# Optimization experiments

Measured on AMD Instinct MI355X. Metric: run time of the kernel, lower is better.

Reference implementation:

```python
import jax, jax.numpy as jnp
import numpy as np

H = 4            # heads
C = 64           # per-head dim (= hidden, PyG TransformerConv semantics)
HD = 64          # hidden_dim
L = 2            # num_layers
NT = 2           # node types: 0=task, 1=machine
ET = ((0, 1), (1, 0))  # edge types: (src_nt, dst_nt)
N = 16384        # nodes per type (== max_nodes -> simple pos-enc slice)
E = 262144       # edges per edge type


def _ln(x, g, b):
    mu = x.mean(-1, keepdims=True)
    var = ((x - mu) ** 2).mean(-1, keepdims=True)
    return (x - mu) * jax.lax.rsqrt(var + 1e-5) * g + b


def _tconv(x_src, x_dst, ei, Wq, bq, Wk, bk, Wv, bv, Ws, bs, Wb):
    # PyG TransformerConv: heads=H, out_channels=C, concat=False, beta=True
    n_dst = x_dst.shape[0]
    src, dst = ei[0], ei[1]
    q = (x_dst @ Wq + bq).reshape(-1, H, C)
    k = (x_src @ Wk + bk).reshape(-1, H, C)
    v = (x_src @ Wv + bv).reshape(-1, H, C)
    logits = jnp.einsum('ehc,ehc->eh', q[dst], k[src]) * (1.0 / float(np.sqrt(C)))  # [E,H]
    m = jax.ops.segment_max(logits, dst, num_segments=n_dst)          # [N,H] segment softmax
    ex = jnp.exp(logits - m[dst])
    denom = jax.ops.segment_sum(ex, dst, num_segments=n_dst)
    alpha = ex / denom[dst]                                            # [E,H]
    msg = (alpha[:, :, None] * v[src]).reshape(-1, H * C)              # [E,H*C]
    out = jax.ops.segment_sum(msg, dst, num_segments=n_dst)
    out = out.reshape(n_dst, H, C).mean(axis=1)                        # concat=False -> head mean
    r = x_dst @ Ws + bs                                                # lin_skip
    beta = jax.nn.sigmoid(jnp.concatenate([out, r, out - r], -1) @ Wb) # lin_beta, [N,1]
    return beta * r + (1.0 - beta) * out


def _forward(edge_index, x, W_in, b_in, type_emb, pos, Wq, bq, Wk, bk, Wv, bv,
             Wskip, bskip, Wbeta, ln_g, ln_b, ff_W1, ff_b1, ff_W2, ff_b2, W_out, b_out):
    # input proj + type embedding + positional encoding (num_nodes == max_nodes -> slice)
    h = [x[t] @ W_in[t] + b_in[t] + type_emb[t] + pos[t] for t in range(NT)]
    for l in range(L):
        hn = [jnp.zeros_like(h[0]), jnp.zeros_like(h[1])]
        for e, (s, d) in enumerate(ET):  # HeteroConv, aggr='sum'
            hn[d] = hn[d] + _tconv(h[s], h[d], edge_index[e],
                                   Wq[l, e], bq[l, e], Wk[l, e], bk[l, e],
                                   Wv[l, e], bv[l, e], Wskip[l, e], bskip[l, e], Wbeta[l, e])
        for t in range(NT):
            hr = _ln(h[t] + hn[t], ln_g[l, t], ln_b[l, t])
            ff = jax.nn.gelu(hr @ ff_W1[l, t] + ff_b1[l, t], approximate=False) @ ff_W2[l, t] + ff_b2[l, t]
            h[t] = hr + ff
    return jnp.stack([h[t] @ W_out[t] + b_out[t] for t in range(NT)])  # [NT,N,HD]


def setup_inputs() -> dict:
    key = jax.random.key(0)
    ks = jax.random.split(key, 16)
    w = lambda k, s: 0.02 * jax.random.normal(k, s, jnp.float32)
    NE = len(ET)
    return {
        'x': jax.random.normal(ks[0], (NT, N, HD), jnp.float32),
        'edge_index': jax.random.randint(ks[1], (NE, 2, E), 0, N, jnp.int32),
        'W_in': w(ks[2], (NT, HD, HD)), 'b_in': jnp.zeros((NT, HD), jnp.float32),
        'type_emb': w(ks[3], (NT, HD)),
        'pos': w(ks[4], (NT, N, HD)),
        'Wq': w(ks[5], (L, NE, HD, H * C)), 'bq': jnp.zeros((L, NE, H * C), jnp.float32),
        'Wk': w(ks[6], (L, NE, HD, H * C)), 'bk': jnp.zeros((L, NE, H * C), jnp.float32),
        'Wv': w(ks[7], (L, NE, HD, H * C)), 'bv': jnp.zeros((L, NE, H * C), jnp.float32),
        'Wskip': w(ks[8], (L, NE, HD, HD)), 'bskip': jnp.zeros((L, NE, HD), jnp.float32),
        'Wbeta': w(ks[9], (L, NE, 3 * HD, 1)),
        'ln_g': jnp.ones((L, NT, HD), jnp.float32), 'ln_b': jnp.zeros((L, NT, HD), jnp.float32),
        'ff_W1': w(ks[10], (L, NT, HD, 4 * HD)), 'ff_b1': jnp.zeros((L, NT, 4 * HD), jnp.float32),
        'ff_W2': w(ks[11], (L, NT, 4 * HD, HD)), 'ff_b2': jnp.zeros((L, NT, HD), jnp.float32),
        'W_out': w(ks[12], (NT, HD, HD)), 'b_out': jnp.zeros((NT, HD), jnp.float32),
    }


def reference(x, edge_index, W_in, b_in, type_emb, pos, Wq, bq, Wk, bk, Wv, bv,
              Wskip, bskip, Wbeta, ln_g, ln_b, ff_W1, ff_b1, ff_W2, ff_b2, W_out, b_out):
    return _forward(edge_index, x, W_in, b_in, type_emb, pos, Wq, bq, Wk, bk, Wv, bv,
                    Wskip, bskip, Wbeta, ln_g, ln_b, ff_W1, ff_b1, ff_W2, ff_b2, W_out, b_out)
```

## Files before the change

kernel.cpp:

```cpp
#include <hip/hip_runtime.h>
#include <math.h>

#define NN 16384
#define EE 262144

typedef __bf16 v8bf __attribute__((ext_vector_type(8)));
typedef __bf16 v4bf __attribute__((ext_vector_type(4)));
typedef float  v4f  __attribute__((ext_vector_type(4)));
typedef float  v2f  __attribute__((ext_vector_type(2)));

#define OFF_CNT     0
#define OFF_FILL    (2*NN)
#define OFF_ROWPTR  (4*NN)
#define OFF_COLSRC  98816
#define OFF_H       623104
#define OFF_HN      (OFF_H  + 2*NN*64)
#define OFF_Q       (OFF_HN + 2*NN*64)
#define OFF_KV      (OFF_Q  + 2*NN*128)
#define OFF_R       (OFF_KV + 2*NN*192)

__device__ __forceinline__ float blo(unsigned u) { return __uint_as_float(u << 16); }
__device__ __forceinline__ float bhi(unsigned u) { return __uint_as_float(u & 0xffff0000u); }
__device__ __forceinline__ unsigned short f2b(float f) {
  __bf16 h = (__bf16)f;
  return *(unsigned short*)&h;
}

__global__ void count_kernel(const int* __restrict__ ei, int* __restrict__ cnt) {
  int idx = blockIdx.x * 256 + threadIdx.x;
  if (idx >= 2 * EE) return;
  int et = idx >> 18;
  int j  = idx & (EE - 1);
  int dst = ei[et * 2 * EE + EE + j];
  atomicAdd(&cnt[et * NN + dst], 1);
}

__global__ __launch_bounds__(1024) void scan_kernel(const int* __restrict__ cnt,
                                                    int* __restrict__ rowptr,
                                                    int* __restrict__ fill) {
  int et = blockIdx.x;
  const int* c = cnt + et * NN;
  __shared__ int sums[1024];
  int tid = threadIdx.x;
  int base = tid * 16;
  int loc[16];
  int s = 0;
#pragma unroll
  for (int i = 0; i < 16; ++i) { loc[i] = s; s += c[base + i]; }
  sums[tid] = s;
  __syncthreads();
  for (int off = 1; off < 1024; off <<= 1) {
    int v = 0;
    if (tid >= off) v = sums[tid - off];
    __syncthreads();
    if (tid >= off) sums[tid] += v;
    __syncthreads();
  }
  int ebase = (tid == 0) ? 0 : sums[tid - 1];
  int* rp = rowptr + et * (NN + 1);
  int* fl = fill + et * NN;
#pragma unroll
  for (int i = 0; i < 16; ++i) {
    rp[base + i] = ebase + loc[i];
    fl[base + i] = ebase + loc[i];
  }
  if (tid == 1023) rp[NN] = sums[1023];
}

__global__ void scatter_kernel(const int* __restrict__ ei, int* __restrict__ fill,
                               int* __restrict__ colsrc) {
  int idx = blockIdx.x * 256 + threadIdx.x;
  if (idx >= 2 * EE) return;
  int et = idx >> 18;
  int j  = idx & (EE - 1);
  int src = ei[et * 2 * EE + j];
  int dst = ei[et * 2 * EE + EE + j];
  int pos = atomicAdd(&fill[et * NN + dst], 1);
  colsrc[et * EE + pos] = (et * NN + src) * 768;
}

struct GemmDesc {
  const float *A, *B, *bias, *bias2, *add;
  char* C;
  int K, Ncols, Cld, tile0, ntiles, gelu, otype;
};
struct GemmPack { GemmDesc d[8]; int nd; };

#define LDA 72

__global__ __launch_bounds__(256) void gemm_mfma(GemmPack p) {
  int y = blockIdx.y;
  int di = 0;
  for (int i = 0; i < p.nd; ++i)
    if (y >= p.d[i].tile0 && y < p.d[i].tile0 + p.d[i].ntiles) di = i;
  GemmDesc g = p.d[di];
  const int col0 = (y - g.tile0) * 64;
  const int row0 = blockIdx.x * 128;
  const int tid = threadIdx.x;
  const int w = tid >> 6, lane = tid & 63;
  const int l16 = lane & 15, quad = lane >> 4;

  __shared__ __bf16 As[128 * LDA];
  __shared__ __bf16 Bs[64 * LDA];

  v4f acc[2][4];
#pragma unroll
  for (int rt = 0; rt < 2; ++rt)
#pragma unroll
    for (int ct = 0; ct < 4; ++ct)
#pragma unroll
      for (int r = 0; r < 4; ++r) acc[rt][ct][r] = 0.f;

  for (int kt = 0; kt < g.K; kt += 64) {
#pragma unroll
    for (int it = 0; it < 8; ++it) {
      int fi = it * 256 + tid;
      int grow = fi >> 4;
      int kq = (fi & 15) << 2;
      float4 a = *(const float4*)(g.A + (size_t)(row0 + grow) * g.K + kt + kq);
      v4bf c = { (__bf16)a.x, (__bf16)a.y, (__bf16)a.z, (__bf16)a.w };
      *(v4bf*)&As[grow * LDA + kq] = c;
    }
#pragma unroll
    for (int it = 0; it < 4; ++it) {
      int fi = it * 256 + tid;
      int kk = fi >> 4;
      int nq = (fi & 15) << 2;
      float4 b = *(const float4*)(g.B + (size_t)(kt + kk) * g.Ncols + col0 + nq);
      Bs[(nq + 0) * LDA + kk] = (__bf16)b.x;
      Bs[(nq + 1) * LDA + kk] = (__bf16)b.y;
      Bs[(nq + 2) * LDA + kk] = (__bf16)b.z;
      Bs[(nq + 3) * LDA + kk] = (__bf16)b.w;
    }
    __syncthreads();
#pragma unroll
    for (int ks = 0; ks < 2; ++ks) {
      v8bf a0 = *(v8bf*)&As[(w * 32 + l16) * LDA + ks * 32 + quad * 8];
      v8bf a1 = *(v8bf*)&As[(w * 32 + 16 + l16) * LDA + ks * 32 + quad * 8];
#pragma unroll
      for (int ct = 0; ct < 4; ++ct) {
        v8bf bb = *(v8bf*)&Bs[(ct * 16 + l16) * LDA + ks * 32 + quad * 8];
        acc[0][ct] = __builtin_amdgcn_mfma_f32_16x16x32_bf16(a0, bb, acc[0][ct], 0, 0, 0);
        acc[1][ct] = __builtin_amdgcn_mfma_f32_16x16x32_bf16(a1, bb, acc[1][ct], 0, 0, 0);
      }
    }
    __syncthreads();
  }

  float bias_c[4];
#pragma unroll
  for (int ct = 0; ct < 4; ++ct) {
    int col = col0 + ct * 16 + l16;
    float b = g.bias ? g.bias[col] : 0.f;
    if (g.bias2) b += g.bias2[col];
    bias_c[ct] = b;
  }
#pragma unroll
  for (int rt = 0; rt < 2; ++rt)
#pragma unroll
    for (int r = 0; r < 4; ++r) {
      size_t row = row0 + w * 32 + rt * 16 + quad * 4 + r;
      char* cp = g.C + row * (size_t)g.Cld;
#pragma unroll
      for (int ct = 0; ct < 4; ++ct) {
        int col = col0 + ct * 16 + l16;
        float v = acc[rt][ct][r] + bias_c[ct];
        if (g.add) v += g.add[row * g.Ncols + col];
        if (g.gelu) v = 0.5f * v * (1.f + erff(v * 0.70710678118654752f));
        if (g.otype == 0)      *(float*)(cp + col * 4) = v;
        else if (g.otype == 1) *(unsigned short*)(cp + col * 2) = f2b(v);
        else {
          unsigned pk = __builtin_amdgcn_cvt_pk_fp8_f32(v, v, 0, false);
          *(unsigned char*)(cp + col) = (unsigned char)(pk & 0xff);
        }
      }
    }
}

struct FFPack {
  const float *HN, *W1, *b1, *W2, *b2;
  float* H;
};

__global__ __launch_bounds__(256) void ff_fused(FFPack p) {
  const int t = blockIdx.y;
  const int row0 = blockIdx.x * 64;
  const int tid = threadIdx.x;
  const int w = tid >> 6, lane = tid & 63;
  const int l16 = lane & 15, quad = lane >> 4;

  const float* A  = p.HN + ((size_t)t * NN) * 64;
  const float* W1 = p.W1 + (size_t)t * 64 * 256;
  const float* b1 = p.b1 + t * 256;
  const float* W2 = p.W2 + (size_t)t * 256 * 64;
  const float* b2 = p.b2 + t * 64;

  __shared__ __bf16 As[64 * LDA];
  __shared__ __bf16 A2[64 * LDA];
  __shared__ __bf16 B1s[64 * LDA];
  __shared__ __bf16 B2s[64 * LDA];

#pragma unroll
  for (int it = 0; it < 4; ++it) {
    int fi = it * 256 + tid;
    int grow = fi >> 4;
    int kq = (fi & 15) << 2;
    float4 a = *(const float4*)(A + (size_t)(row0 + grow) * 64 + kq);
    v4bf c = { (__bf16)a.x, (__bf16)a.y, (__bf16)a.z, (__bf16)a.w };
    *(v4bf*)&As[grow * LDA + kq] = c;
  }

  v4f acc2[4];
#pragma unroll
  for (int ct = 0; ct < 4; ++ct)
#pragma unroll
    for (int r = 0; r < 4; ++r) acc2[ct][r] = 0.f;

  for (int c1 = 0; c1 < 4; ++c1) {
#pragma unroll
    for (int it = 0; it < 4; ++it) {
      int fi = it * 256 + tid;
      int kk = fi >> 4;
      int nq = (fi & 15) << 2;
      float4 b = *(const float4*)(W1 + (size_t)kk * 256 + c1 * 64 + nq);
      B1s[(nq + 0) * LDA + kk] = (__bf16)b.x;
      B1s[(nq + 1) * LDA + kk] = (__bf16)b.y;
      B1s[(nq + 2) * LDA + kk] = (__bf16)b.z;
      B1s[(nq + 3) * LDA + kk] = (__bf16)b.w;
      float4 b2v = *(const float4*)(W2 + (size_t)(c1 * 64 + kk) * 64 + nq);
      B2s[(nq + 0) * LDA + kk] = (__bf16)b2v.x;
      B2s[(nq + 1) * LDA + kk] = (__bf16)b2v.y;
      B2s[(nq + 2) * LDA + kk] = (__bf16)b2v.z;
      B2s[(nq + 3) * LDA + kk] = (__bf16)b2v.w;
    }
    __syncthreads();

    v4f acc1[4];
#pragma unroll
    for (int ct = 0; ct < 4; ++ct)
#pragma unroll
      for (int r = 0; r < 4; ++r) acc1[ct][r] = 0.f;
#pragma unroll
    for (int ks = 0; ks < 2; ++ks) {
      v8bf a = *(v8bf*)&As[(w * 16 + l16) * LDA + ks * 32 + quad * 8];
#pragma unroll
      for (int ct = 0; ct < 4; ++ct) {
        v8bf bb = *(v8bf*)&B1s[(ct * 16 + l16) * LDA + ks * 32 + quad * 8];
        acc1[ct] = __builtin_amdgcn_mfma_f32_16x16x32_bf16(a, bb, acc1[ct], 0, 0, 0);
      }
    }
#pragma unroll
    for (int ct = 0; ct < 4; ++ct) {
      float bb = b1[c1 * 64 + ct * 16 + l16];
#pragma unroll
      for (int r = 0; r < 4; ++r) {
        float v = acc1[ct][r] + bb;
        v = 0.5f * v * (1.f + erff(v * 0.70710678118654752f));
        A2[(w * 16 + quad * 4 + r) * LDA + ct * 16 + l16] = (__bf16)v;
      }
    }
#pragma unroll
    for (int ks = 0; ks < 2; ++ks) {
      v8bf a = *(v8bf*)&A2[(w * 16 + l16) * LDA + ks * 32 + quad * 8];
#pragma unroll
      for (int ct = 0; ct < 4; ++ct) {
        v8bf bb = *(v8bf*)&B2s[(ct * 16 + l16) * LDA + ks * 32 + quad * 8];
        acc2[ct] = __builtin_amdgcn_mfma_f32_16x16x32_bf16(a, bb, acc2[ct], 0, 0, 0);
      }
    }
    __syncthreads();
  }

#pragma unroll
  for (int ct = 0; ct < 4; ++ct) {
    int col = ct * 16 + l16;
    float bb = b2[col];
#pragma unroll
    for (int r = 0; r < 4; ++r) {
      size_t row = (size_t)t * NN + row0 + w * 16 + quad * 4 + r;
      float v = acc2[ct][r] + bb + p.HN[row * 64 + col];
      p.H[row * 64 + col] = v;
    }
  }
}

struct AggPack {
  const unsigned short *Q;
  const char *KV;
  const float *R;
  const float *Wb;
  const float *Hin;
  const float *lng, *lnb;
  float* outHR;
  const int *rowptr;
  const int *colsrc;
};

__global__ __launch_bounds__(256) void agg_kernel(AggPack p) {
  const int et = blockIdx.y, d = 1 - et;
  int wid = __builtin_amdgcn_readfirstlane(threadIdx.x >> 6);
  int lane = threadIdx.x & 63;
  int node = blockIdx.x * 4 + wid;
  int c4 = lane & 15;
  int cb = ((lane >> 4) << 6) + (c4 << 2);

  const int* rp = p.rowptr + et * (NN + 1);
  const int* cs = p.colsrc + et * EE;
  int start = rp[node], end = rp[node + 1];
  int len = end - start;
  int gnode = d * NN + node;

  uint2 qw = *(const uint2*)(p.Q + ((size_t)gnode << 8) + cb);
  float q0 = blo(qw.x) * 0.125f, q1 = bhi(qw.x) * 0.125f;
  float q2 = blo(qw.y) * 0.125f, q3 = bhi(qw.y) * 0.125f;

  int b[5];
#pragma unroll
  for (int i = 0; i <= 4; ++i) b[i] = start + ((len * i) >> 2);
  float dsum[4] = {0.f, 0.f, 0.f, 0.f};
  float acc[4][4];
#pragma unroll
  for (int s4 = 0; s4 < 4; ++s4)
#pragma unroll
    for (int c = 0; c < 4; ++c) acc[s4][c] = 0.f;

  int maxn = (len + 3) >> 2;
  int last = end - 1;
  for (int it = 0; it < maxn; ++it) {
#pragma unroll
    for (int s4 = 0; s4 < 4; ++s4) {
      int j = b[s4] + it;
      bool act = j < b[s4 + 1];
      int jc = act ? j : last;
      int off = cs[jc];
      const char* rowp = p.KV + off;
      unsigned kw = *(const unsigned*)(rowp + cb);
      uint2 vw = *(const uint2*)(rowp + 256 + cb * 2);
      v2f kl = __builtin_amdgcn_cvt_pk_f32_fp8((int)kw, false);
      v2f kh = __builtin_amdgcn_cvt_pk_f32_fp8((int)kw, true);
      float pd = q0 * kl[0] + q1 * kl[1] + q2 * kh[0] + q3 * kh[1];
      pd += __shfl_xor(pd, 1);
      pd += __shfl_xor(pd, 2);
      pd += __shfl_xor(pd, 4);
      pd += __shfl_xor(pd, 8);
      float wgt = act ? __expf(pd) : 0.f;
      dsum[s4] += wgt;
      acc[s4][0] += wgt * blo(vw.x);
      acc[s4][1] += wgt * bhi(vw.x);
      acc[s4][2] += wgt * blo(vw.y);
      acc[s4][3] += wgt * bhi(vw.y);
    }
  }
  float dn = (dsum[0] + dsum[1]) + (dsum[2] + dsum[3]);
  float ax = (acc[0][0] + acc[1][0]) + (acc[2][0] + acc[3][0]);
  float ay = (acc[0][1] + acc[1][1]) + (acc[2][1] + acc[3][1]);
  float az = (acc[0][2] + acc[1][2]) + (acc[2][2] + acc[3][2]);
  float aw = (acc[0][3] + acc[1][3]) + (acc[2][3] + acc[3][3]);

  float inv = (len > 0) ? (0.25f / dn) : 0.f;
  float ox = ax * inv, oy = ay * inv, oz = az * inv, ow = aw * inv;
  ox += __shfl_xor(ox, 16); ox += __shfl_xor(ox, 32);
  oy += __shfl_xor(oy, 16); oy += __shfl_xor(oy, 32);
  oz += __shfl_xor(oz, 16); oz += __shfl_xor(oz, 32);
  ow += __shfl_xor(ow, 16); ow += __shfl_xor(ow, 32);

  int cc = c4 << 2;
  float4 r = *(const float4*)(p.R + (size_t)gnode * 64 + cc);
  const float* wb = p.Wb + et * 192;
  float part = ox * wb[cc] + oy * wb[cc + 1] + oz * wb[cc + 2] + ow * wb[cc + 3]
             + r.x * wb[64 + cc] + r.y * wb[64 + cc + 1]
             + r.z * wb[64 + cc + 2] + r.w * wb[64 + cc + 3]
             + (ox - r.x) * wb[128 + cc] + (oy - r.y) * wb[128 + cc + 1]
             + (oz - r.z) * wb[128 + cc + 2] + (ow - r.w) * wb[128 + cc + 3];
  part += __shfl_xor(part, 1);
  part += __shfl_xor(part, 2);
  part += __shfl_xor(part, 4);
  part += __shfl_xor(part, 8);
  float beta = 1.f / (1.f + __expf(-part));

  float4 hv = *(const float4*)(p.Hin + (size_t)gnode * 64 + cc);
  float yx = hv.x + beta * r.x + (1.f - beta) * ox;
  float yy = hv.y + beta * r.y + (1.f - beta) * oy;
  float yz = hv.z + beta * r.z + (1.f - beta) * oz;
  float yw = hv.w + beta * r.w + (1.f - beta) * ow;
  float sa = yx + yy + yz + yw;
  float sb = yx * yx + yy * yy + yz * yz + yw * yw;
  sa += __shfl_xor(sa, 1); sb += __shfl_xor(sb, 1);
  sa += __shfl_xor(sa, 2); sb += __shfl_xor(sb, 2);
  sa += __shfl_xor(sa, 4); sb += __shfl_xor(sb, 4);
  sa += __shfl_xor(sa, 8); sb += __shfl_xor(sb, 8);
  float mu = sa * (1.f / 64.f);
  float var = sb * (1.f / 64.f) - mu * mu;
  float rs = rsqrtf(var + 1e-5f);
  if (lane < 16) {
    const float* lng = p.lng + d * 64;
    const float* lnb = p.lnb + d * 64;
    float4 gg = *(const float4*)(lng + cc);
    float4 bb = *(const float4*)(lnb + cc);
    float4 res;
    res.x = (yx - mu) * rs * gg.x + bb.x;
    res.y = (yy - mu) * rs * gg.y + bb.y;
    res.z = (yz - mu) * rs * gg.z + bb.z;
    res.w = (yw - mu) * rs * gg.w + bb.w;
    *(float4*)(p.outHR + (size_t)gnode * 64 + cc) = res;
  }
}

static void add_desc(GemmPack& p, int& tiles, const float* A, const float* B,
                     const float* bias, const float* bias2, const float* add,
                     void* C, int K, int Nc, int Cld, int gelu, int otype) {
  GemmDesc& g = p.d[p.nd++];
  g.A = A; g.B = B; g.bias = bias; g.bias2 = bias2; g.add = add; g.C = (char*)C;
  g.K = K; g.Ncols = Nc; g.Cld = Cld; g.tile0 = tiles; g.ntiles = Nc / 64;
  g.gelu = gelu; g.otype = otype;
  tiles += g.ntiles;
}

extern "C" void kernel_launch(void* const* d_in, const int* in_sizes, int n_in,
                              void* d_out, int out_size, void* d_ws, size_t ws_size,
                              hipStream_t stream) {
  const float* x        = (const float*)d_in[0];
  const int*   ei       = (const int*)d_in[1];
  const float* W_in     = (const float*)d_in[2];
  const float* b_in     = (const float*)d_in[3];
  const float* type_emb = (const float*)d_in[4];
  const float* pos      = (const float*)d_in[5];
  const float* Wq       = (const float*)d_in[6];
  const float* bq       = (const float*)d_in[7];
  const float* Wk       = (const float*)d_in[8];
  const float* bk       = (const float*)d_in[9];
  const float* Wv       = (const float*)d_in[10];
  const float* bv       = (const float*)d_in[11];
  const float* Wskip    = (const float*)d_in[12];
  const float* bskip    = (const float*)d_in[13];
  const float* Wbeta    = (const float*)d_in[14];
  const float* ln_g     = (const float*)d_in[15];
  const float* ln_b     = (const float*)d_in[16];
  const float* ff_W1    = (const float*)d_in[17];
  const float* ff_b1    = (const float*)d_in[18];
  const float* ff_W2    = (const float*)d_in[19];
  const float* ff_b2    = (const float*)d_in[20];
  const float* W_out    = (const float*)d_in[21];
  const float* b_out    = (const float*)d_in[22];
  float* out = (float*)d_out;

  int*   wsi = (int*)d_ws;
  float* wsf = (float*)d_ws;
  int* cnt    = wsi + OFF_CNT;
  int* fill   = wsi + OFF_FILL;
  int* rowptr = wsi + OFF_ROWPTR;
  int* colsrc = wsi + OFF_COLSRC;
  float* H  = wsf + OFF_H;
  float* HN = wsf + OFF_HN;
  unsigned short* Qb = (unsigned short*)(wsf + OFF_Q);
  char* KVb = (char*)(wsf + OFF_KV);
  float* Rb = wsf + OFF_R;

  hipMemsetAsync(cnt, 0, 2 * NN * sizeof(int), stream);
  count_kernel<<<dim3(2 * EE / 256), dim3(256), 0, stream>>>(ei, cnt);
  scan_kernel<<<dim3(2), dim3(1024), 0, stream>>>(cnt, rowptr, fill);
  scatter_kernel<<<dim3(2 * EE / 256), dim3(256), 0, stream>>>(ei, fill, colsrc);

  {
    GemmPack p{}; int tiles = 0;
    for (int t = 0; t < 2; ++t)
      add_desc(p, tiles, x + (size_t)t * NN * 64, W_in + t * 64 * 64,
               b_in + t * 64, type_emb + t * 64, pos + (size_t)t * NN * 64,
               H + (size_t)t * NN * 64, 64, 64, 256, 0, 0);
    gemm_mfma<<<dim3(128, tiles), dim3(256), 0, stream>>>(p);
  }

  for (int l = 0; l < 2; ++l) {
    {
      GemmPack p{}; int tiles = 0;
      for (int et = 0; et < 2; ++et) {
        int s = et, d = 1 - et;
        int we = l * 2 + et;
        const float* hs = H + (size_t)s * NN * 64;
        const float* hd = H + (size_t)d * NN * 64;
        add_desc(p, tiles, hd, Wq + (size_t)we * 64 * 256, bq + we * 256,
                 nullptr, nullptr, (char*)Qb + (size_t)d * NN * 512, 64, 256, 512, 0, 1);
        add_desc(p, tiles, hs, Wk + (size_t)we * 64 * 256, bk + we * 256,
                 nullptr, nullptr, KVb + (size_t)s * NN * 768, 64, 256, 768, 0, 2);
        add_desc(p, tiles, hs, Wv + (size_t)we * 64 * 256, bv + we * 256,
                 nullptr, nullptr, KVb + (size_t)s * NN * 768 + 256, 64, 256, 768, 0, 1);
        add_desc(p, tiles, hd, Wskip + (size_t)we * 64 * 64, bskip + we * 64,
                 nullptr, nullptr, Rb + (size_t)d * NN * 64, 64, 64, 256, 0, 0);
      }
      gemm_mfma<<<dim3(128, tiles), dim3(256), 0, stream>>>(p);
    }

    AggPack ap;
    ap.Q = Qb; ap.KV = KVb; ap.R = Rb;
    ap.Wb = Wbeta + l * 2 * 192;
    ap.Hin = H;
    ap.lng = ln_g + l * 128;
    ap.lnb = ln_b + l * 128;
    ap.outHR = HN;
    ap.rowptr = rowptr;
    ap.colsrc = colsrc;
    agg_kernel<<<dim3(NN / 4, 2), dim3(256), 0, stream>>>(ap);

    FFPack fp;
    fp.HN = HN;
    fp.W1 = ff_W1 + (size_t)l * 2 * 64 * 256;
    fp.b1 = ff_b1 + l * 2 * 256;
    fp.W2 = ff_W2 + (size_t)l * 2 * 256 * 64;
    fp.b2 = ff_b2 + l * 2 * 64;
    fp.H  = H;
    ff_fused<<<dim3(NN / 64, 2), dim3(256), 0, stream>>>(fp);
  }

  {
    GemmPack p{}; int tiles = 0;
    for (int t = 0; t < 2; ++t)
      add_desc(p, tiles, H + (size_t)t * NN * 64, W_out + t * 64 * 64,
               b_out + t * 64, nullptr, nullptr,
               out + (size_t)t * NN * 64, 64, 64, 256, 0, 0);
    gemm_mfma<<<dim3(128, tiles), dim3(256), 0, stream>>>(p);
  }
}
```

Baseline: 394.6 us.

## Reuse staged A tile across column tiles in GEMM; widen per-lane aggregation to 8 channels

The packed GEMM now launches one block per descriptor and row tile, stages the A rows into LDS once, and loops over all 64-column output tiles. Before, each column tile re-read and re-converted A. This cuts repeated global reads of the input activations but makes far fewer blocks (grid y shrinks from 26 to 8 in the projection launch) and serializes column tiles within a block. The aggregation kernel switches each lane to 8 channels with two half-waves processing two edge segments each. That gives wider K/V loads and fewer shuffle steps, at the cost of more registers per lane.

```diff
diff --git a/kernel.cpp b/kernel.cpp
--- a/kernel.cpp
+++ b/kernel.cpp
@@ -82,19 +82,14 @@
 struct GemmDesc {
   const float *A, *B, *bias, *bias2, *add;
   char* C;
-  int K, Ncols, Cld, tile0, ntiles, gelu, otype;
+  int Ncols, Cld, ntiles, gelu, otype;
 };
 struct GemmPack { GemmDesc d[8]; int nd; };
 
 #define LDA 72
 
 __global__ __launch_bounds__(256) void gemm_mfma(GemmPack p) {
-  int y = blockIdx.y;
-  int di = 0;
-  for (int i = 0; i < p.nd; ++i)
-    if (y >= p.d[i].tile0 && y < p.d[i].tile0 + p.d[i].ntiles) di = i;
-  GemmDesc g = p.d[di];
-  const int col0 = (y - g.tile0) * 64;
+  GemmDesc g = p.d[blockIdx.y];
   const int row0 = blockIdx.x * 128;
   const int tid = threadIdx.x;
   const int w = tid >> 6, lane = tid & 63;
@@ -103,36 +98,40 @@
   __shared__ __bf16 As[128 * LDA];
   __shared__ __bf16 Bs[64 * LDA];
 
-  v4f acc[2][4];
-#pragma unroll
-  for (int rt = 0; rt < 2; ++rt)
-#pragma unroll
-    for (int ct = 0; ct < 4; ++ct)
-#pragma unroll
-      for (int r = 0; r < 4; ++r) acc[rt][ct][r] = 0.f;
-
-  for (int kt = 0; kt < g.K; kt += 64) {
-#pragma unroll
-    for (int it = 0; it < 8; ++it) {
-      int fi = it * 256 + tid;
-      int grow = fi >> 4;
-      int kq = (fi & 15) << 2;
-      float4 a = *(const float4*)(g.A + (size_t)(row0 + grow) * g.K + kt + kq);
-      v4bf c = { (__bf16)a.x, (__bf16)a.y, (__bf16)a.z, (__bf16)a.w };
-      *(v4bf*)&As[grow * LDA + kq] = c;
-    }
+#pragma unroll
+  for (int it = 0; it < 8; ++it) {
+    int fi = it * 256 + tid;
+    int grow = fi >> 4;
+    int kq = (fi & 15) << 2;
+    float4 a = *(const float4*)(g.A + (size_t)(row0 + grow) * 64 + kq);
+    v4bf c = { (__bf16)a.x, (__bf16)a.y, (__bf16)a.z, (__bf16)a.w };
+    *(v4bf*)&As[grow * LDA + kq] = c;
+  }
+
+  for (int ct0 = 0; ct0 < g.ntiles; ++ct0) {
+    const int col0 = ct0 * 64;
+    __syncthreads();
 #pragma unroll
     for (int it = 0; it < 4; ++it) {
       int fi = it * 256 + tid;
       int kk = fi >> 4;
       int nq = (fi & 15) << 2;
-      float4 b = *(const float4*)(g.B + (size_t)(kt + kk) * g.Ncols + col0 + nq);
+      float4 b = *(const float4*)(g.B + (size_t)kk * g.Ncols + col0 + nq);
       Bs[(nq + 0) * LDA + kk] = (__bf16)b.x;
       Bs[(nq + 1) * LDA + kk] = (__bf16)b.y;
       Bs[(nq + 2) * LDA + kk] = (__bf16)b.z;
       Bs[(nq + 3) * LDA + kk] = (__bf16)b.w;
     }
     __syncthreads();
+
+    v4f acc[2][4];
+#pragma unroll
+    for (int rt = 0; rt < 2; ++rt)
+#pragma unroll
+      for (int ct = 0; ct < 4; ++ct)
+#pragma unroll
+        for (int r = 0; r < 4; ++r) acc[rt][ct][r] = 0.f;
+
 #pragma unroll
     for (int ks = 0; ks < 2; ++ks) {
       v8bf a0 = *(v8bf*)&As[(w * 32 + l16) * LDA + ks * 32 + quad * 8];
@@ -144,37 +143,36 @@
         acc[1][ct] = __builtin_amdgcn_mfma_f32_16x16x32_bf16(a1, bb, acc[1][ct], 0, 0, 0);
       }
     }
-    __syncthreads();
-  }
-
-  float bias_c[4];
-#pragma unroll
-  for (int ct = 0; ct < 4; ++ct) {
-    int col = col0 + ct * 16 + l16;
-    float b = g.bias ? g.bias[col] : 0.f;
-    if (g.bias2) b += g.bias2[col];
-    bias_c[ct] = b;
-  }
-#pragma unroll
-  for (int rt = 0; rt < 2; ++rt)
-#pragma unroll
-    for (int r = 0; r < 4; ++r) {
-      size_t row = row0 + w * 32 + rt * 16 + quad * 4 + r;
-      char* cp = g.C + row * (size_t)g.Cld;
-#pragma unroll
-      for (int ct = 0; ct < 4; ++ct) {
-        int col = col0 + ct * 16 + l16;
-        float v = acc[rt][ct][r] + bias_c[ct];
-        if (g.add) v += g.add[row * g.Ncols + col];
-        if (g.gelu) v = 0.5f * v * (1.f + erff(v * 0.70710678118654752f));
-        if (g.otype == 0)      *(float*)(cp + col * 4) = v;
-        else if (g.otype == 1) *(unsigned short*)(cp + col * 2) = f2b(v);
-        else {
-          unsigned pk = __builtin_amdgcn_cvt_pk_fp8_f32(v, v, 0, false);
-          *(unsigned char*)(cp + col) = (unsigned char)(pk & 0xff);
+
+    float bias_c[4];
+#pragma unroll
+    for (int ct = 0; ct < 4; ++ct) {
+      int col = col0 + ct * 16 + l16;
+      float b = g.bias ? g.bias[col] : 0.f;
+      if (g.bias2) b += g.bias2[col];
+      bias_c[ct] = b;
+    }
+#pragma unroll
+    for (int rt = 0; rt < 2; ++rt)
+#pragma unroll
+      for (int r = 0; r < 4; ++r) {
+        size_t row = row0 + w * 32 + rt * 16 + quad * 4 + r;
+        char* cp = g.C + row * (size_t)g.Cld;
+#pragma unroll
+        for (int ct = 0; ct < 4; ++ct) {
+          int col = col0 + ct * 16 + l16;
+          float v = acc[rt][ct][r] + bias_c[ct];
+          if (g.add) v += g.add[row * g.Ncols + col];
+          if (g.gelu) v = 0.5f * v * (1.f + erff(v * 0.70710678118654752f));
+          if (g.otype == 0)      *(float*)(cp + col * 4) = v;
+          else if (g.otype == 1) *(unsigned short*)(cp + col * 2) = f2b(v);
+          else {
+            unsigned pk = __builtin_amdgcn_cvt_pk_fp8_f32(v, v, 0, false);
+            *(unsigned char*)(cp + col) = (unsigned char)(pk & 0xff);
+          }
         }
       }
-    }
+  }
 }
 
 struct FFPack {
@@ -301,8 +299,10 @@
   int wid = __builtin_amdgcn_readfirstlane(threadIdx.x >> 6);
   int lane = threadIdx.x & 63;
   int node = blockIdx.x * 4 + wid;
-  int c4 = lane & 15;
-  int cb = ((lane >> 4) << 6) + (c4 << 2);
+  int lane5 = lane & 31;
+  int sub = lane >> 5;
+  int c8 = lane5 & 7;
+  int cb8 = ((lane5 >> 3) << 6) + (c8 << 3);
 
   const int* rp = p.rowptr + et * (NN + 1);
   const int* cs = p.colsrc + et * EE;
@@ -310,110 +310,141 @@
   int len = end - start;
   int gnode = d * NN + node;
 
-  uint2 qw = *(const uint2*)(p.Q + ((size_t)gnode << 8) + cb);
-  float q0 = blo(qw.x) * 0.125f, q1 = bhi(qw.x) * 0.125f;
-  float q2 = blo(qw.y) * 0.125f, q3 = bhi(qw.y) * 0.125f;
+  float q[8];
+  {
+    uint4 qw = *(const uint4*)(p.Q + ((size_t)gnode << 8) + cb8);
+    q[0] = blo(qw.x) * 0.125f; q[1] = bhi(qw.x) * 0.125f;
+    q[2] = blo(qw.y) * 0.125f; q[3] = bhi(qw.y) * 0.125f;
+    q[4] = blo(qw.z) * 0.125f; q[5] = bhi(qw.z) * 0.125f;
+    q[6] = blo(qw.w) * 0.125f; q[7] = bhi(qw.w) * 0.125f;
+  }
 
   int b[5];
 #pragma unroll
   for (int i = 0; i <= 4; ++i) b[i] = start + ((len * i) >> 2);
-  float dsum[4] = {0.f, 0.f, 0.f, 0.f};
-  float acc[4][4];
-#pragma unroll
-  for (int s4 = 0; s4 < 4; ++s4)
-#pragma unroll
-    for (int c = 0; c < 4; ++c) acc[s4][c] = 0.f;
+  int s0lo = sub ? b[2] : b[0];
+  int s0hi = sub ? b[3] : b[1];
+  int s1lo = sub ? b[3] : b[1];
+  int s1hi = sub ? b[4] : b[2];
+
+  float dsum[2] = {0.f, 0.f};
+  float acc[2][8];
+#pragma unroll
+  for (int u = 0; u < 2; ++u)
+#pragma unroll
+    for (int i = 0; i < 8; ++i) acc[u][i] = 0.f;
 
   int maxn = (len + 3) >> 2;
   int last = end - 1;
   for (int it = 0; it < maxn; ++it) {
 #pragma unroll
-    for (int s4 = 0; s4 < 4; ++s4) {
-      int j = b[s4] + it;
-      bool act = j < b[s4 + 1];
+    for (int u = 0; u < 2; ++u) {
+      int jlo = u ? s1lo : s0lo;
+      int jhi = u ? s1hi : s0hi;
+      int j = jlo + it;
+      bool act = j < jhi;
       int jc = act ? j : last;
       int off = cs[jc];
       const char* rowp = p.KV + off;
-      unsigned kw = *(const unsigned*)(rowp + cb);
-      uint2 vw = *(const uint2*)(rowp + 256 + cb * 2);
-      v2f kl = __builtin_amdgcn_cvt_pk_f32_fp8((int)kw, false);
-      v2f kh = __builtin_amdgcn_cvt_pk_f32_fp8((int)kw, true);
-      float pd = q0 * kl[0] + q1 * kl[1] + q2 * kh[0] + q3 * kh[1];
+      uint2 kw = *(const uint2*)(rowp + cb8);
+      uint4 vw = *(const uint4*)(rowp + 256 + cb8 * 2);
+      v2f k0 = __builtin_amdgcn_cvt_pk_f32_fp8((int)kw.x, false);
+      v2f k1 = __builtin_amdgcn_cvt_pk_f32_fp8((int)kw.x, true);
+      v2f k2 = __builtin_amdgcn_cvt_pk_f32_fp8((int)kw.y, false);
+      v2f k3 = __builtin_amdgcn_cvt_pk_f32_fp8((int)kw.y, true);
+      float pd = q[0] * k0[0] + q[1] * k0[1] + q[2] * k1[0] + q[3] * k1[1]
+               + q[4] * k2[0] + q[5] * k2[1] + q[6] * k3[0] + q[7] * k3[1];
       pd += __shfl_xor(pd, 1);
       pd += __shfl_xor(pd, 2);
       pd += __shfl_xor(pd, 4);
-      pd += __shfl_xor(pd, 8);
       float wgt = act ? __expf(pd) : 0.f;
-      dsum[s4] += wgt;
-      acc[s4][0] += wgt * blo(vw.x);
-      acc[s4][1] += wgt * bhi(vw.x);
-      acc[s4][2] += wgt * blo(vw.y);
-      acc[s4][3] += wgt * bhi(vw.y);
-    }
-  }
-  float dn = (dsum[0] + dsum[1]) + (dsum[2] + dsum[3]);
-  float ax = (acc[0][0] + acc[1][0]) + (acc[2][0] + acc[3][0]);
-  float ay = (acc[0][1] + acc[1][1]) + (acc[2][1] + acc[3][1]);
-  float az = (acc[0][2] + acc[1][2]) + (acc[2][2] + acc[3][2]);
-  float aw = (acc[0][3] + acc[1][3]) + (acc[2][3] + acc[3][3]);
-
+      dsum[u] += wgt;
+      acc[u][0] += wgt * blo(vw.x); acc[u][1] += wgt * bhi(vw.x);
+      acc[u][2] += wgt * blo(vw.y); acc[u][3] += wgt * bhi(vw.y);
+      acc[u][4] += wgt * blo(vw.z); acc[u][5] += wgt * bhi(vw.z);
+      acc[u][6] += wgt * blo(vw.w); acc[u][7] += wgt * bhi(vw.w);
+    }
+  }
+
+  float dn = dsum[0] + dsum[1];
+  dn += __shfl_xor(dn, 32);
+  float o[8];
+#pragma unroll
+  for (int i = 0; i < 8; ++i) {
+    float a = acc[0][i] + acc[1][i];
+    a += __shfl_xor(a, 32);
+    o[i] = a;
+  }
   float inv = (len > 0) ? (0.25f / dn) : 0.f;
-  float ox = ax * inv, oy = ay * inv, oz = az * inv, ow = aw * inv;
-  ox += __shfl_xor(ox, 16); ox += __shfl_xor(ox, 32);
-  oy += __shfl_xor(oy, 16); oy += __shfl_xor(oy, 32);
-  oz += __shfl_xor(oz, 16); oz += __shfl_xor(oz, 32);
-  ow += __shfl_xor(ow, 16); ow += __shfl_xor(ow, 32);
-
-  int cc = c4 << 2;
-  float4 r = *(const float4*)(p.R + (size_t)gnode * 64 + cc);
+#pragma unroll
+  for (int i = 0; i < 8; ++i) {
+    float v = o[i] * inv;
+    v += __shfl_xor(v, 8);
+    v += __shfl_xor(v, 16);
+    o[i] = v;
+  }
+
+  int cc = c8 << 3;
   const float* wb = p.Wb + et * 192;
-  float part = ox * wb[cc] + oy * wb[cc + 1] + oz * wb[cc + 2] + ow * wb[cc + 3]
-             + r.x * wb[64 + cc] + r.y * wb[64 + cc + 1]
-             + r.z * wb[64 + cc + 2] + r.w * wb[64 + cc + 3]
-             + (ox - r.x) * wb[128 + cc] + (oy - r.y) * wb[128 + cc + 1]
-             + (oz - r.z) * wb[128 + cc + 2] + (ow - r.w) * wb[128 + cc + 3];
+  float4 w0a = *(const float4*)(wb + cc),       w0b = *(const float4*)(wb + cc + 4);
+  float4 w1a = *(const float4*)(wb + 64 + cc),  w1b = *(const float4*)(wb + 64 + cc + 4);
+  float4 w2a = *(const float4*)(wb + 128 + cc), w2b = *(const float4*)(wb + 128 + cc + 4);
+  float4 ra = *(const float4*)(p.R + (size_t)gnode * 64 + cc);
+  float4 rb = *(const float4*)(p.R + (size_t)gnode * 64 + cc + 4);
+  float r[8] = {ra.x, ra.y, ra.z, ra.w, rb.x, rb.y, rb.z, rb.w};
+  float wb0[8] = {w0a.x, w0a.y, w0a.z, w0a.w, w0b.x, w0b.y, w0b.z, w0b.w};
+  float wb1[8] = {w1a.x, w1a.y, w1a.z, w1a.w, w1b.x, w1b.y, w1b.z, w1b.w};
+  float wb2[8] = {w2a.x, w2a.y, w2a.z, w2a.w, w2b.x, w2b.y, w2b.z, w2b.w};
+
+  float part = 0.f;
+#pragma unroll
+  for (int i = 0; i < 8; ++i)
+    part += o[i] * wb0[i] + r[i] * wb1[i] + (o[i] - r[i]) * wb2[i];
   part += __shfl_xor(part, 1);
   part += __shfl_xor(part, 2);
   part += __shfl_xor(part, 4);
-  part += __shfl_xor(part, 8);
   float beta = 1.f / (1.f + __expf(-part));
 
-  float4 hv = *(const float4*)(p.Hin + (size_t)gnode * 64 + cc);
-  float yx = hv.x + beta * r.x + (1.f - beta) * ox;
-  float yy = hv.y + beta * r.y + (1.f - beta) * oy;
-  float yz = hv.z + beta * r.z + (1.f - beta) * oz;
-  float yw = hv.w + beta * r.w + (1.f - beta) * ow;
-  float sa = yx + yy + yz + yw;
-  float sb = yx * yx + yy * yy + yz * yz + yw * yw;
+  float4 ha = *(const float4*)(p.Hin + (size_t)gnode * 64 + cc);
+  float4 hb = *(const float4*)(p.Hin + (size_t)gnode * 64 + cc + 4);
+  float hv[8] = {ha.x, ha.y, ha.z, ha.w, hb.x, hb.y, hb.z, hb.w};
+  float y[8];
+  float sa = 0.f, sb = 0.f;
+#pragma unroll
+  for (int i = 0; i < 8; ++i) {
+    y[i] = hv[i] + beta * r[i] + (1.f - beta) * o[i];
+    sa += y[i];
+    sb += y[i] * y[i];
+  }
   sa += __shfl_xor(sa, 1); sb += __shfl_xor(sb, 1);
   sa += __shfl_xor(sa, 2); sb += __shfl_xor(sb, 2);
   sa += __shfl_xor(sa, 4); sb += __shfl_xor(sb, 4);
-  sa += __shfl_xor(sa, 8); sb += __shfl_xor(sb, 8);
   float mu = sa * (1.f / 64.f);
   float var = sb * (1.f / 64.f) - mu * mu;
   float rs = rsqrtf(var + 1e-5f);
-  if (lane < 16) {
+  if (lane < 8) {
     const float* lng = p.lng + d * 64;
     const float* lnb = p.lnb + d * 64;
-    float4 gg = *(const float4*)(lng + cc);
-    float4 bb = *(const float4*)(lnb + cc);
-    float4 res;
-    res.x = (yx - mu) * rs * gg.x + bb.x;
-    res.y = (yy - mu) * rs * gg.y + bb.y;
-    res.z = (yz - mu) * rs * gg.z + bb.z;
-    res.w = (yw - mu) * rs * gg.w + bb.w;
-    *(float4*)(p.outHR + (size_t)gnode * 64 + cc) = res;
-  }
-}
-
-static void add_desc(GemmPack& p, int& tiles, const float* A, const float* B,
+    float4 ga = *(const float4*)(lng + cc), gb = *(const float4*)(lng + cc + 4);
+    float4 ba = *(const float4*)(lnb + cc), bbv = *(const float4*)(lnb + cc + 4);
+    float gg[8] = {ga.x, ga.y, ga.z, ga.w, gb.x, gb.y, gb.z, gb.w};
+    float bbx[8] = {ba.x, ba.y, ba.z, ba.w, bbv.x, bbv.y, bbv.z, bbv.w};
+    float res[8];
+#pragma unroll
+    for (int i = 0; i < 8; ++i) res[i] = (y[i] - mu) * rs * gg[i] + bbx[i];
+    float* op = p.outHR + (size_t)gnode * 64 + cc;
+    *(float4*)op = make_float4(res[0], res[1], res[2], res[3]);
+    *(float4*)(op + 4) = make_float4(res[4], res[5], res[6], res[7]);
+  }
+}
+
+static void add_desc(GemmPack& p, const float* A, const float* B,
                      const float* bias, const float* bias2, const float* add,
-                     void* C, int K, int Nc, int Cld, int gelu, int otype) {
+                     void* C, int Nc, int Cld, int gelu, int otype) {
   GemmDesc& g = p.d[p.nd++];
   g.A = A; g.B = B; g.bias = bias; g.bias2 = bias2; g.add = add; g.C = (char*)C;
-  g.K = K; g.Ncols = Nc; g.Cld = Cld; g.tile0 = tiles; g.ntiles = Nc / 64;
+  g.Ncols = Nc; g.Cld = Cld; g.ntiles = Nc / 64;
   g.gelu = gelu; g.otype = otype;
-  tiles += g.ntiles;
 }
 
 extern "C" void kernel_launch(void* const* d_in, const int* in_sizes, int n_in,
@@ -462,32 +493,32 @@
   scatter_kernel<<<dim3(2 * EE / 256), dim3(256), 0, stream>>>(ei, fill, colsrc);
 
   {
-    GemmPack p{}; int tiles = 0;
+    GemmPack p{};
     for (int t = 0; t < 2; ++t)
-      add_desc(p, tiles, x + (size_t)t * NN * 64, W_in + t * 64 * 64,
+      add_desc(p, x + (size_t)t * NN * 64, W_in + t * 64 * 64,
                b_in + t * 64, type_emb + t * 64, pos + (size_t)t * NN * 64,
-               H + (size_t)t * NN * 64, 64, 64, 256, 0, 0);
-    gemm_mfma<<<dim3(128, tiles), dim3(256), 0, stream>>>(p);
+               H + (size_t)t * NN * 64, 64, 256, 0, 0);
+    gemm_mfma<<<dim3(128, p.nd), dim3(256), 0, stream>>>(p);
   }
 
   for (int l = 0; l < 2; ++l) {
     {
-      GemmPack p{}; int tiles = 0;
+      GemmPack p{};
       for (int et = 0; et < 2; ++et) {
         int s = et, d = 1 - et;
         int we = l * 2 + et;
         const float* hs = H + (size_t)s * NN * 64;
         const float* hd = H + (size_t)d * NN * 64;
-        add_desc(p, tiles, hd, Wq + (size_t)we * 64 * 256, bq + we * 256,
-                 nullptr, nullptr, (char*)Qb + (size_t)d * NN * 512, 64, 256, 512, 0, 1);
-        add_desc(p, tiles, hs, Wk + (size_t)we * 64 * 256, bk + we * 256,
-                 nullptr, nullptr, KVb + (size_t)s * NN * 768, 64, 256, 768, 0, 2);
-        add_desc(p, tiles, hs, Wv + (size_t)we * 64 * 256, bv + we * 256,
-                 nullptr, nullptr, KVb + (size_t)s * NN * 768 + 256, 64, 256, 768, 0, 1);
-        add_desc(p, tiles, hd, Wskip + (size_t)we * 64 * 64, bskip + we * 64,
-                 nullptr, nullptr, Rb + (size_t)d * NN * 64, 64, 64, 256, 0, 0);
+        add_desc(p, hd, Wq + (size_t)we * 64 * 256, bq + we * 256,
+                 nullptr, nullptr, (char*)Qb + (size_t)d * NN * 512, 256, 512, 0, 1);
+        add_desc(p, hs, Wk + (size_t)we * 64 * 256, bk + we * 256,
+                 nullptr, nullptr, KVb + (size_t)s * NN * 768, 256, 768, 0, 2);
+        add_desc(p, hs, Wv + (size_t)we * 64 * 256, bv + we * 256,
+                 nullptr, nullptr, KVb + (size_t)s * NN * 768 + 256, 256, 768, 0, 1);
+        add_desc(p, hd, Wskip + (size_t)we * 64 * 64, bskip + we * 64,
+                 nullptr, nullptr, Rb + (size_t)d * NN * 64, 64, 256, 0, 0);
       }
-      gemm_mfma<<<dim3(128, tiles), dim3(256), 0, stream>>>(p);
+      gemm_mfma<<<dim3(128, p.nd), dim3(256), 0, stream>>>(p);
     }
 
     AggPack ap;
@@ -512,11 +543,11 @@
   }
 
   {
-    GemmPack p{}; int tiles = 0;
+    GemmPack p{};
     for (int t = 0; t < 2; ++t)
-      add_desc(p, tiles, H + (size_t)t * NN * 64, W_out + t * 64 * 64,
+      add_desc(p, H + (size_t)t * NN * 64, W_out + t * 64 * 64,
                b_out + t * 64, nullptr, nullptr,
-               out + (size_t)t * NN * 64, 64, 64, 256, 0, 0);
-    gemm_mfma<<<dim3(128, tiles), dim3(256), 0, stream>>>(p);
-  }
-}
+               out + (size_t)t * NN * 64, 64, 256, 0, 0);
+    gemm_mfma<<<dim3(128, p.nd), dim3(256), 0, stream>>>(p);
+  }
+}
```

Result: no change. 401.7 us (+1.8%).

## Reuse A tile across column tiles in GEMM and fuse output projection into FF

Applied to the files above, without the earlier changes.

The grouped GEMM now launches one block per descriptor instead of per 64-column tile. Each block loads and converts its 128-row A tile once, then loops over all column tiles, which removes redundant A reads for the wide Q/K/V projections. Separately, the final layer's FF kernel keeps the residual output in shared memory and applies the output projection there, so the last GEMM launch and the write and re-read of H are gone. The cost is fewer blocks in the QKV GEMM (8x128 instead of 26x128) and serialized column tiles per block, which can lower parallelism.

```diff
diff --git a/kernel.cpp b/kernel.cpp
--- a/kernel.cpp
+++ b/kernel.cpp
@@ -82,19 +82,14 @@
 struct GemmDesc {
   const float *A, *B, *bias, *bias2, *add;
   char* C;
-  int K, Ncols, Cld, tile0, ntiles, gelu, otype;
+  int Ncols, Cld, ntiles, gelu, otype;
 };
 struct GemmPack { GemmDesc d[8]; int nd; };
 
 #define LDA 72
 
 __global__ __launch_bounds__(256) void gemm_mfma(GemmPack p) {
-  int y = blockIdx.y;
-  int di = 0;
-  for (int i = 0; i < p.nd; ++i)
-    if (y >= p.d[i].tile0 && y < p.d[i].tile0 + p.d[i].ntiles) di = i;
-  GemmDesc g = p.d[di];
-  const int col0 = (y - g.tile0) * 64;
+  GemmDesc g = p.d[blockIdx.y];
   const int row0 = blockIdx.x * 128;
   const int tid = threadIdx.x;
   const int w = tid >> 6, lane = tid & 63;
@@ -103,36 +98,40 @@
   __shared__ __bf16 As[128 * LDA];
   __shared__ __bf16 Bs[64 * LDA];
 
-  v4f acc[2][4];
-#pragma unroll
-  for (int rt = 0; rt < 2; ++rt)
-#pragma unroll
-    for (int ct = 0; ct < 4; ++ct)
-#pragma unroll
-      for (int r = 0; r < 4; ++r) acc[rt][ct][r] = 0.f;
-
-  for (int kt = 0; kt < g.K; kt += 64) {
-#pragma unroll
-    for (int it = 0; it < 8; ++it) {
-      int fi = it * 256 + tid;
-      int grow = fi >> 4;
-      int kq = (fi & 15) << 2;
-      float4 a = *(const float4*)(g.A + (size_t)(row0 + grow) * g.K + kt + kq);
-      v4bf c = { (__bf16)a.x, (__bf16)a.y, (__bf16)a.z, (__bf16)a.w };
-      *(v4bf*)&As[grow * LDA + kq] = c;
-    }
+#pragma unroll
+  for (int it = 0; it < 8; ++it) {
+    int fi = it * 256 + tid;
+    int grow = fi >> 4;
+    int kq = (fi & 15) << 2;
+    float4 a = *(const float4*)(g.A + (size_t)(row0 + grow) * 64 + kq);
+    v4bf c = { (__bf16)a.x, (__bf16)a.y, (__bf16)a.z, (__bf16)a.w };
+    *(v4bf*)&As[grow * LDA + kq] = c;
+  }
+
+  for (int ct0 = 0; ct0 < g.ntiles; ++ct0) {
+    const int col0 = ct0 * 64;
+    __syncthreads();
 #pragma unroll
     for (int it = 0; it < 4; ++it) {
       int fi = it * 256 + tid;
       int kk = fi >> 4;
       int nq = (fi & 15) << 2;
-      float4 b = *(const float4*)(g.B + (size_t)(kt + kk) * g.Ncols + col0 + nq);
+      float4 b = *(const float4*)(g.B + (size_t)kk * g.Ncols + col0 + nq);
       Bs[(nq + 0) * LDA + kk] = (__bf16)b.x;
       Bs[(nq + 1) * LDA + kk] = (__bf16)b.y;
       Bs[(nq + 2) * LDA + kk] = (__bf16)b.z;
       Bs[(nq + 3) * LDA + kk] = (__bf16)b.w;
     }
     __syncthreads();
+
+    v4f acc[2][4];
+#pragma unroll
+    for (int rt = 0; rt < 2; ++rt)
+#pragma unroll
+      for (int ct = 0; ct < 4; ++ct)
+#pragma unroll
+        for (int r = 0; r < 4; ++r) acc[rt][ct][r] = 0.f;
+
 #pragma unroll
     for (int ks = 0; ks < 2; ++ks) {
       v8bf a0 = *(v8bf*)&As[(w * 32 + l16) * LDA + ks * 32 + quad * 8];
@@ -144,42 +143,43 @@
         acc[1][ct] = __builtin_amdgcn_mfma_f32_16x16x32_bf16(a1, bb, acc[1][ct], 0, 0, 0);
       }
     }
-    __syncthreads();
-  }
-
-  float bias_c[4];
-#pragma unroll
-  for (int ct = 0; ct < 4; ++ct) {
-    int col = col0 + ct * 16 + l16;
-    float b = g.bias ? g.bias[col] : 0.f;
-    if (g.bias2) b += g.bias2[col];
-    bias_c[ct] = b;
-  }
-#pragma unroll
-  for (int rt = 0; rt < 2; ++rt)
-#pragma unroll
-    for (int r = 0; r < 4; ++r) {
-      size_t row = row0 + w * 32 + rt * 16 + quad * 4 + r;
-      char* cp = g.C + row * (size_t)g.Cld;
-#pragma unroll
-      for (int ct = 0; ct < 4; ++ct) {
-        int col = col0 + ct * 16 + l16;
-        float v = acc[rt][ct][r] + bias_c[ct];
-        if (g.add) v += g.add[row * g.Ncols + col];
-        if (g.gelu) v = 0.5f * v * (1.f + erff(v * 0.70710678118654752f));
-        if (g.otype == 0)      *(float*)(cp + col * 4) = v;
-        else if (g.otype == 1) *(unsigned short*)(cp + col * 2) = f2b(v);
-        else {
-          unsigned pk = __builtin_amdgcn_cvt_pk_fp8_f32(v, v, 0, false);
-          *(unsigned char*)(cp + col) = (unsigned char)(pk & 0xff);
+
+    float bias_c[4];
+#pragma unroll
+    for (int ct = 0; ct < 4; ++ct) {
+      int col = col0 + ct * 16 + l16;
+      float b = g.bias ? g.bias[col] : 0.f;
+      if (g.bias2) b += g.bias2[col];
+      bias_c[ct] = b;
+    }
+#pragma unroll
+    for (int rt = 0; rt < 2; ++rt)
+#pragma unroll
+      for (int r = 0; r < 4; ++r) {
+        size_t row = row0 + w * 32 + rt * 16 + quad * 4 + r;
+        char* cp = g.C + row * (size_t)g.Cld;
+#pragma unroll
+        for (int ct = 0; ct < 4; ++ct) {
+          int col = col0 + ct * 16 + l16;
+          float v = acc[rt][ct][r] + bias_c[ct];
+          if (g.add) v += g.add[row * g.Ncols + col];
+          if (g.gelu) v = 0.5f * v * (1.f + erff(v * 0.70710678118654752f));
+          if (g.otype == 0)      *(float*)(cp + col * 4) = v;
+          else if (g.otype == 1) *(unsigned short*)(cp + col * 2) = f2b(v);
+          else {
+            unsigned pk = __builtin_amdgcn_cvt_pk_fp8_f32(v, v, 0, false);
+            *(unsigned char*)(cp + col) = (unsigned char)(pk & 0xff);
+          }
         }
       }
-    }
+  }
 }
 
 struct FFPack {
   const float *HN, *W1, *b1, *W2, *b2;
   float* H;
+  const float *Wout, *bout;
+  float* outbuf;
 };
 
 __global__ __launch_bounds__(256) void ff_fused(FFPack p) {
@@ -271,15 +271,72 @@
     __syncthreads();
   }
 
+  if (!p.outbuf) {
+#pragma unroll
+    for (int ct = 0; ct < 4; ++ct) {
+      int col = ct * 16 + l16;
+      float bb = b2[col];
+#pragma unroll
+      for (int r = 0; r < 4; ++r) {
+        size_t row = (size_t)t * NN + row0 + w * 16 + quad * 4 + r;
+        float v = acc2[ct][r] + bb + p.HN[row * 64 + col];
+        p.H[row * 64 + col] = v;
+      }
+    }
+    return;
+  }
+
 #pragma unroll
   for (int ct = 0; ct < 4; ++ct) {
     int col = ct * 16 + l16;
     float bb = b2[col];
 #pragma unroll
     for (int r = 0; r < 4; ++r) {
+      int lrow = w * 16 + quad * 4 + r;
+      size_t row = (size_t)t * NN + row0 + lrow;
+      float v = acc2[ct][r] + bb + p.HN[row * 64 + col];
+      A2[lrow * LDA + col] = (__bf16)v;
+    }
+  }
+  {
+    const float* Wo = p.Wout + (size_t)t * 64 * 64;
+#pragma unroll
+    for (int it = 0; it < 4; ++it) {
+      int fi = it * 256 + tid;
+      int kk = fi >> 4;
+      int nq = (fi & 15) << 2;
+      float4 b = *(const float4*)(Wo + (size_t)kk * 64 + nq);
+      B1s[(nq + 0) * LDA + kk] = (__bf16)b.x;
+      B1s[(nq + 1) * LDA + kk] = (__bf16)b.y;
+      B1s[(nq + 2) * LDA + kk] = (__bf16)b.z;
+      B1s[(nq + 3) * LDA + kk] = (__bf16)b.w;
+    }
+  }
+  __syncthreads();
+
+  v4f acc3[4];
+#pragma unroll
+  for (int ct = 0; ct < 4; ++ct)
+#pragma unroll
+    for (int r = 0; r < 4; ++r) acc3[ct][r] = 0.f;
+#pragma unroll
+  for (int ks = 0; ks < 2; ++ks) {
+    v8bf a = *(v8bf*)&A2[(w * 16 + l16) * LDA + ks * 32 + quad * 8];
+#pragma unroll
+    for (int ct = 0; ct < 4; ++ct) {
+      v8bf bb = *(v8bf*)&B1s[(ct * 16 + l16) * LDA + ks * 32 + quad * 8];
+      acc3[ct] = __builtin_amdgcn_mfma_f32_16x16x32_bf16(a, bb, acc3[ct], 0, 0, 0);
+    }
+  }
+  const float* bo = p.bout + t * 64;
+#pragma unroll
+  for (int ct = 0; ct < 4; ++ct) {
+    int col = ct * 16 + l16;
+    float bb = bo[col];
+#pragma unroll
+    for (int r = 0; r < 4; ++r) {
       size_t row = (size_t)t * NN + row0 + w * 16 + quad * 4 + r;
-      float v = acc2[ct][r] + bb + p.HN[row * 64 + col];
-      p.H[row * 64 + col] = v;
+      p.outbuf[row * 64 + col] = acc3[ct][r] + bb;
     }
   }
 }
@@ -406,14 +463,13 @@
   }
 }
 
-static void add_desc(GemmPack& p, int& tiles, const float* A, const float* B,
+static void add_desc(GemmPack& p, const float* A, const float* B,
                      const float* bias, const float* bias2, const float* add,
-                     void* C, int K, int Nc, int Cld, int gelu, int otype) {
+                     void* C, int Nc, int Cld, int gelu, int otype) {
   GemmDesc& g = p.d[p.nd++];
   g.A = A; g.B = B; g.bias = bias; g.bias2 = bias2; g.add = add; g.C = (char*)C;
-  g.K = K; g.Ncols = Nc; g.Cld = Cld; g.tile0 = tiles; g.ntiles = Nc / 64;
+  g.Ncols = Nc; g.Cld = Cld; g.ntiles = Nc / 64;
   g.gelu = gelu; g.otype = otype;
-  tiles += g.ntiles;
 }
 
 extern "C" void kernel_launch(void* const* d_in, const int* in_sizes, int n_in,
@@ -462,32 +518,32 @@
   scatter_kernel<<<dim3(2 * EE / 256), dim3(256), 0, stream>>>(ei, fill, colsrc);
 
   {
-    GemmPack p{}; int tiles = 0;
+    GemmPack p{};
     for (int t = 0; t < 2; ++t)
-      add_desc(p, tiles, x + (size_t)t * NN * 64, W_in + t * 64 * 64,
+      add_desc(p, x + (size_t)t * NN * 64, W_in + t * 64 * 64,
                b_in + t * 64, type_emb + t * 64, pos + (size_t)t * NN * 64,
-               H + (size_t)t * NN * 64, 64, 64, 256, 0, 0);
-    gemm_mfma<<<dim3(128, tiles), dim3(256), 0, stream>>>(p);
+               H + (size_t)t * NN * 64, 64, 256, 0, 0);
+    gemm_mfma<<<dim3(128, p.nd), dim3(256), 0, stream>>>(p);
   }
 
   for (int l = 0; l < 2; ++l) {
     {
-      GemmPack p{}; int tiles = 0;
+      GemmPack p{};
       for (int et = 0; et < 2; ++et) {
         int s = et, d = 1 - et;
         int we = l * 2 + et;
         const float* hs = H + (size_t)s * NN * 64;
         const float* hd = H + (size_t)d * NN * 64;
-        add_desc(p, tiles, hd, Wq + (size_t)we * 64 * 256, bq + we * 256,
-                 nullptr, nullptr, (char*)Qb + (size_t)d * NN * 512, 64, 256, 512, 0, 1);
-        add_desc(p, tiles, hs, Wk + (size_t)we * 64 * 256, bk + we * 256,
-                 nullptr, nullptr, KVb + (size_t)s * NN * 768, 64, 256, 768, 0, 2);
-        add_desc(p, tiles, hs, Wv + (size_t)we * 64 * 256, bv + we * 256,
-                 nullptr, nullptr, KVb + (size_t)s * NN * 768 + 256, 64, 256, 768, 0, 1);
-        add_desc(p, tiles, hd, Wskip + (size_t)we * 64 * 64, bskip + we * 64,
-                 nullptr, nullptr, Rb + (size_t)d * NN * 64, 64, 64, 256, 0, 0);
-      }
-      gemm_mfma<<<dim3(128, tiles), dim3(256), 0, stream>>>(p);
+        add_desc(p, hd, Wq + (size_t)we * 64 * 256, bq + we * 256,
+                 nullptr, nullptr, (char*)Qb + (size_t)d * NN * 512, 256, 512, 0, 1);
+        add_desc(p, hs, Wk + (size_t)we * 64 * 256, bk + we * 256,
+                 nullptr, nullptr, KVb + (size_t)s * NN * 768, 256, 768, 0, 2);
+        add_desc(p, hs, Wv + (size_t)we * 64 * 256, bv + we * 256,
+                 nullptr, nullptr, KVb + (size_t)s * NN * 768 + 256, 256, 768, 0, 1);
+        add_desc(p, hd, Wskip + (size_t)we * 64 * 64, bskip + we * 64,
+                 nullptr, nullptr, Rb + (size_t)d * NN * 64, 64, 256, 0, 0);
+      }
+      gemm_mfma<<<dim3(128, p.nd), dim3(256), 0, stream>>>(p);
     }
 
     AggPack ap;
@@ -508,15 +564,9 @@
     fp.W2 = ff_W2 + (size_t)l * 2 * 256 * 64;
     fp.b2 = ff_b2 + l * 2 * 64;
     fp.H  = H;
+    fp.Wout = W_out;
+    fp.bout = b_out;
+    fp.outbuf = (l == 1) ? out : nullptr;
     ff_fused<<<dim3(NN / 64, 2), dim3(256), 0, stream>>>(fp);
   }
-
-  {
-    GemmPack p{}; int tiles = 0;
-    for (int t = 0; t < 2; ++t)
-      add_desc(p, tiles, H + (size_t)t * NN * 64, W_out + t * 64 * 64,
-               b_out + t * 64, nullptr, nullptr,
-               out + (size_t)t * NN * 64, 64, 64, 256, 0, 0);
-    gemm_mfma<<<dim3(128, tiles), dim3(256), 0, stream>>>(p);
-  }
-}
+}
```

Result: faster. 385.8 us (-2.2%).
